# Kernel tuning notes

Hardware: AMD Instinct MI355X
Metric: run time of the kernel (lower is better)

Reference implementation:

```python
import jax, jax.numpy as jnp
import numpy as np


def _unit(h):
    # F.normalize(p=2, dim=-1) equivalent (NormalizeFunc 'unit')
    n = jnp.sqrt(jnp.sum(h * h, axis=-1, keepdims=True))
    return h / jnp.maximum(n, 1e-12)


def setup_inputs() -> dict:
    key = jax.random.key(0)
    k = jax.random.split(key, 6)
    B, T, D, size = 48, 32, 1024, 512
    x = jax.random.normal(k[0], (B, T, D), dtype=jnp.float32)
    w_leaf = jax.random.normal(k[1], (D, size), dtype=jnp.float32) / np.sqrt(D)
    b_leaf = jnp.zeros((size,), dtype=jnp.float32)
    w_comp = jax.random.normal(k[2], (2 * size, size), dtype=jnp.float32) / np.sqrt(2 * size)
    b_comp = jnp.zeros((size,), dtype=jnp.float32)
    s_bilinear = jax.random.normal(k[3], (size, size), dtype=jnp.float32) / np.sqrt(size)
    return {"x": x, "w_leaf": w_leaf, "b_leaf": b_leaf,
            "w_comp": w_comp, "b_comp": b_comp, "s_bilinear": s_bilinear}


def reference(x, w_leaf, b_leaf, w_comp, b_comp, s_bilinear):
    B, T, D = x.shape
    size = w_leaf.shape[1]
    # chart offsets: level lv occupies offsets[lv] : offsets[lv] + (T - lv)
    offsets = np.concatenate([[0], np.cumsum(T - np.arange(T))]).astype(np.int64)
    ncells = T * (T + 1) // 2

    # leaf_transform: MLP + unit normalization
    leaf = _unit(jax.nn.relu(x @ w_leaf + b_leaf))  # [B, T, size]
    chart_h = jnp.zeros((B, ncells, size), x.dtype).at[:, :T].set(leaf)
    chart_s = jnp.zeros((B, ncells, 1), x.dtype)

    for level in range(1, T):
        L = T - level  # spans at this level
        N = level      # split points per span
        pos = np.arange(L)[:, None]
        n = np.arange(N)[None, :]
        # left child: level n at pos; right child: level (level-n-1) at pos+n+1
        l_idx = offsets[n] + pos                       # [L, N]
        r_idx = offsets[level - n - 1] + pos + n + 1   # [L, N]

        lh = chart_h[:, l_idx]  # [B, L, N, size]
        rh = chart_h[:, r_idx]  # [B, L, N, size]
        ls = chart_s[:, l_idx]  # [B, L, N, 1]
        rs = chart_s[:, r_idx]  # [B, L, N, 1]

        # inside_compose: MLP over concatenated children
        h = jax.nn.relu(jnp.concatenate([lh, rh], axis=-1) @ w_comp + b_comp)
        # inside_score: bilinear compatibility
        xs = jnp.einsum('blnd,de,blne->bln', lh, s_bilinear, rh)[..., None]
        s = xs + ls + rs                  # [B, L, N, 1]
        p = jax.nn.softmax(s, axis=2)
        hbar = _unit(jnp.sum(h * p, axis=2))  # [B, L, size]
        sbar = jnp.sum(s * p, axis=2)         # [B, L, 1]

        off = int(offsets[level])
        chart_h = chart_h.at[:, off:off + L].set(hbar)
        chart_s = chart_s.at[:, off:off + L].set(sbar)

    return chart_h
```

## Files before the change

### kernel.cpp

```cpp
#include <hip/hip_runtime.h>
#include <math.h>

#define BB 48
#define TT 32
#define DD 1024
#define SZ 512
#define NCELLS 528

typedef unsigned short u16;
typedef unsigned int u32;
typedef __attribute__((ext_vector_type(8))) short bf16x8;
typedef __attribute__((ext_vector_type(4))) float f32x4;

__device__ __forceinline__ int off_of(int k) { return TT * k - (k * (k - 1)) / 2; }

__device__ __forceinline__ u16 f2bf(float x) {
    u32 u = __float_as_uint(x);
    u32 r = (u + 0x7fffu + ((u >> 16) & 1u)) >> 16;
    return (u16)r;
}
__device__ __forceinline__ float bf2f(u16 h) {
    return __uint_as_float(((u32)h) << 16);
}
__device__ __forceinline__ u32 pack2(u16 a, u16 b) {
    return (u32)a | ((u32)b << 16);
}
__device__ __forceinline__ float2 upk(u32 v) {
    return make_float2(__uint_as_float(v << 16),
                       __uint_as_float(v & 0xffff0000u));
}

__global__ __launch_bounds__(256) void prep_w(
    const float* __restrict__ w_comp, const float* __restrict__ s_bil,
    u16* __restrict__ WT)
{
    int idx = blockIdx.x * 256 + threadIdx.x;
    int n = idx >> 9, k = idx & 511;
    float w;
    if (n < 512)       w = w_comp[(size_t)k * SZ + n];
    else if (n < 1024) w = w_comp[(size_t)(512 + k) * SZ + (n - 512)];
    else               w = s_bil[(size_t)k * SZ + (n - 1024)];
    WT[idx] = f2bf(w);
}

__global__ __launch_bounds__(256) void prep_wl(
    const float* __restrict__ w_leaf,
    u16* __restrict__ WLT_hi, u16* __restrict__ WLT_lo)
{
    int idx = blockIdx.x * 256 + threadIdx.x;
    int n = idx >> 10, k = idx & 1023;
    float w = w_leaf[(size_t)k * SZ + n];
    u16 hi = f2bf(w);
    u16 lo = f2bf(w - bf2f(hi));
    WLT_hi[idx] = hi;
    WLT_lo[idx] = lo;
}

__global__ __launch_bounds__(256) void leaf_mfma(
    const float* __restrict__ x,
    const u16* __restrict__ WLT_hi, const u16* __restrict__ WLT_lo,
    const float* __restrict__ b_leaf, float* __restrict__ leaf_pre)
{
    __shared__ u16 Ah[128][40];
    __shared__ u16 Bh[64][40], Bl[64][40];

    const int col0 = blockIdx.x * 64;
    const int row0 = blockIdx.y * 128;
    const int t = threadIdx.x;

    const int srow = t >> 1, skh = (t & 1) * 16;
    const float* ap = x + (size_t)(row0 + srow) * DD + skh;
    const int bcol = t >> 2, bch = (t & 3) * 8;
    const u16* bph = WLT_hi + (size_t)(col0 + bcol) * DD + bch;
    const u16* bpl = WLT_lo + (size_t)(col0 + bcol) * DD + bch;

    const int lane = t & 63, wv = t >> 6;
    const int wr = wv >> 1, wc = wv & 1;
    const int l15 = lane & 15, lko = (lane >> 4) * 8;

    f32x4 acc[4][2];
    #pragma unroll
    for (int i = 0; i < 4; ++i)
        #pragma unroll
        for (int j = 0; j < 2; ++j)
            #pragma unroll
            for (int e = 0; e < 4; ++e) acc[i][j][e] = 0.f;

    float4 pa[4];
    uint4 pbh, pbl;
    #pragma unroll
    for (int c = 0; c < 4; ++c) pa[c] = *(const float4*)(ap + c * 4);
    pbh = *(const uint4*)bph;
    pbl = *(const uint4*)bpl;

    for (int k0 = 0; k0 < DD; k0 += 32) {
        u32 wh[8];
        #pragma unroll
        for (int c = 0; c < 4; ++c) {
            wh[c * 2]     = pack2(f2bf(pa[c].x), f2bf(pa[c].y));
            wh[c * 2 + 1] = pack2(f2bf(pa[c].z), f2bf(pa[c].w));
        }
        *(uint4*)&Ah[srow][skh]     = make_uint4(wh[0], wh[1], wh[2], wh[3]);
        *(uint4*)&Ah[srow][skh + 8] = make_uint4(wh[4], wh[5], wh[6], wh[7]);
        *(uint4*)&Bh[bcol][bch] = pbh;
        *(uint4*)&Bl[bcol][bch] = pbl;
        __syncthreads();

        if (k0 + 32 < DD) {
            #pragma unroll
            for (int c = 0; c < 4; ++c)
                pa[c] = *(const float4*)(ap + k0 + 32 + c * 4);
            pbh = *(const uint4*)(bph + k0 + 32);
            pbl = *(const uint4*)(bpl + k0 + 32);
        }

        bf16x8 fah[4], fbh[2], fbl[2];
        #pragma unroll
        for (int i = 0; i < 4; ++i)
            fah[i] = *(const bf16x8*)&Ah[wr * 64 + i * 16 + l15][lko];
        #pragma unroll
        for (int j = 0; j < 2; ++j) {
            fbh[j] = *(const bf16x8*)&Bh[wc * 32 + j * 16 + l15][lko];
            fbl[j] = *(const bf16x8*)&Bl[wc * 32 + j * 16 + l15][lko];
        }
        #pragma unroll
        for (int i = 0; i < 4; ++i) {
            #pragma unroll
            for (int j = 0; j < 2; ++j) {
                acc[i][j] = __builtin_amdgcn_mfma_f32_16x16x32_bf16(
                    fah[i], fbh[j], acc[i][j], 0, 0, 0);
                acc[i][j] = __builtin_amdgcn_mfma_f32_16x16x32_bf16(
                    fah[i], fbl[j], acc[i][j], 0, 0, 0);
            }
        }
        __syncthreads();
    }

    #pragma unroll
    for (int i = 0; i < 4; ++i) {
        int rbase = row0 + wr * 64 + i * 16 + (lane >> 4) * 4;
        #pragma unroll
        for (int j = 0; j < 2; ++j) {
            int gc = col0 + wc * 32 + j * 16 + l15;
            float bc = b_leaf[gc];
            #pragma unroll
            for (int q = 0; q < 4; ++q)
                leaf_pre[(size_t)(rbase + q) * SZ + gc] =
                    fmaxf(acc[i][j][q] + bc, 0.f);
        }
    }
}

__global__ __launch_bounds__(256) void leaf_norm(
    const float* __restrict__ leaf_pre, float* __restrict__ chart_h,
    u16* __restrict__ Hchart, float* __restrict__ Sarr)
{
    const int r = blockIdx.x;
    const int b = r >> 5, pos = r & 31;
    const int cell = b * NCELLS + pos;
    const int t = threadIdx.x, lane = t & 63, wave = t >> 6;
    __shared__ float red[4];

    float2 v = *(const float2*)&leaf_pre[(size_t)r * SZ + 2 * t];
    float sq = v.x * v.x + v.y * v.y;
    #pragma unroll
    for (int o = 32; o; o >>= 1) sq += __shfl_xor(sq, o);
    if (lane == 0) red[wave] = sq;
    __syncthreads();
    float nrm = sqrtf(red[0] + red[1] + red[2] + red[3]);
    float inv = 1.f / fmaxf(nrm, 1e-12f);
    v.x *= inv; v.y *= inv;
    *(float2*)&chart_h[(size_t)cell * SZ + 2 * t] = v;
    ((u32*)Hchart)[(size_t)cell * 256 + t] = pack2(f2bf(v.x), f2bf(v.y));
    if (t == 0) Sarr[cell] = 0.f;
}

__global__ __launch_bounds__(256) void transform_mfma(
    const u16* __restrict__ Hchart, const u16* __restrict__ WT,
    const float* __restrict__ b_comp,
    u16* __restrict__ ACU, int level, int nrt)
{
    __shared__ u16 Ah[64][40];
    __shared__ u16 Bh[64][40];
    __shared__ int cidx[64];

    const int L = TT - level, rows = BB * L, off = off_of(level);
    const int id = blockIdx.x;
    const int w = (id & 7) * (3 * nrt) + (id >> 3);
    const int rt = w / 24, ct = w % 24;
    const int col0 = ct * 64;

    const int t = threadIdx.x;
    if (t < 64) {
        int g = rt * 64 + t;
        cidx[t] = (g < rows) ? ((g / L) * NCELLS + off + (g % L)) : -1;
    }

    const int srow = t >> 2, skc = (t & 3) * 8;
    int ga = rt * 64 + srow;
    if (ga >= rows) ga = rows - 1;
    const int acell = (ga / L) * NCELLS + off + (ga % L);
    const u16* aph = Hchart + (size_t)acell * SZ + skc;
    const u16* bph = WT + (size_t)(col0 + srow) * SZ + skc;

    const int lane = t & 63, wv = t >> 6;
    const int wr = wv >> 1, wc = wv & 1;
    const int l15 = lane & 15, lko = (lane >> 4) * 8;

    f32x4 acc[2][2];
    #pragma unroll
    for (int i = 0; i < 2; ++i)
        #pragma unroll
        for (int j = 0; j < 2; ++j)
            #pragma unroll
            for (int e = 0; e < 4; ++e) acc[i][j][e] = 0.f;

    uint4 pah = *(const uint4*)aph;
    uint4 pbh = *(const uint4*)bph;

    for (int k0 = 0; k0 < SZ; k0 += 32) {
        *(uint4*)&Ah[srow][skc] = pah;
        *(uint4*)&Bh[srow][skc] = pbh;
        __syncthreads();

        if (k0 + 32 < SZ) {
            pah = *(const uint4*)(aph + k0 + 32);
            pbh = *(const uint4*)(bph + k0 + 32);
        }

        bf16x8 fah[2], fbh[2];
        #pragma unroll
        for (int i = 0; i < 2; ++i)
            fah[i] = *(const bf16x8*)&Ah[wr * 32 + i * 16 + l15][lko];
        #pragma unroll
        for (int j = 0; j < 2; ++j)
            fbh[j] = *(const bf16x8*)&Bh[wc * 32 + j * 16 + l15][lko];
        #pragma unroll
        for (int i = 0; i < 2; ++i)
            #pragma unroll
            for (int j = 0; j < 2; ++j)
                acc[i][j] = __builtin_amdgcn_mfma_f32_16x16x32_bf16(
                    fah[i], fbh[j], acc[i][j], 0, 0, 0);
        __syncthreads();
    }

    #pragma unroll
    for (int i = 0; i < 2; ++i) {
        int rbase = wr * 32 + i * 16 + (lane >> 4) * 4;
        #pragma unroll
        for (int j = 0; j < 2; ++j) {
            int gc = col0 + wc * 32 + j * 16 + l15;
            float bias = (gc < 512) ? b_comp[gc] : 0.f;
            #pragma unroll
            for (int q = 0; q < 4; ++q) {
                int ci = cidx[rbase + q];
                if (ci >= 0)
                    ACU[(size_t)ci * 1536 + gc] = f2bf(acc[i][j][q] + bias);
            }
        }
    }
}

__global__ __launch_bounds__(512) void combine_kernel(
    float* __restrict__ chart_h, const u16* __restrict__ ACU,
    const u16* __restrict__ Hchart,
    float* __restrict__ Sarr, u16* __restrict__ Hchart_w, int level)
{
    const int L = TT - level, N = level;
    const int cpx = (BB * L) >> 3;
    const int swz = (blockIdx.x & 7) * cpx + (blockIdx.x >> 3);
    const int b = swz / L, pos = swz % L;
    const int off = off_of(level);

    __shared__ float s_lds[32], p_lds[32], spre[32];
    __shared__ int lcell[32], rcell[32];
    __shared__ float hred[8][512];
    __shared__ float red[8];

    const int t = threadIdx.x, lane = t & 63, wv = t >> 6;

    if (t < N) {
        int lc = b * NCELLS + off_of(t) + pos;
        int rc = b * NCELLS + off_of(level - t - 1) + pos + t + 1;
        lcell[t] = lc;
        rcell[t] = rc;
        spre[t] = Sarr[lc] + Sarr[rc];
    }
    __syncthreads();

    for (int n = wv; n < N; n += 8) {
        const u16* u  = ACU + (size_t)lcell[n] * 1536 + 1024;
        const u16* hr = Hchart + (size_t)rcell[n] * SZ;
        uint4 uv = *(const uint4*)&u[lane * 8];
        uint4 hv = *(const uint4*)&hr[lane * 8];
        float d = 0.f;
        {
            float2 a = upk(uv.x), h2 = upk(hv.x);
            d = fmaf(a.x, h2.x, fmaf(a.y, h2.y, d));
        }
        {
            float2 a = upk(uv.y), h2 = upk(hv.y);
            d = fmaf(a.x, h2.x, fmaf(a.y, h2.y, d));
        }
        {
            float2 a = upk(uv.z), h2 = upk(hv.z);
            d = fmaf(a.x, h2.x, fmaf(a.y, h2.y, d));
        }
        {
            float2 a = upk(uv.w), h2 = upk(hv.w);
            d = fmaf(a.x, h2.x, fmaf(a.y, h2.y, d));
        }
        #pragma unroll
        for (int o = 32; o; o >>= 1) d += __shfl_xor(d, o);
        if (lane == 0) s_lds[n] = d + spre[n];
    }
    __syncthreads();

    if (wv == 0) {
        float sv = (lane < N) ? s_lds[lane] : -INFINITY;
        float m = sv;
        #pragma unroll
        for (int o = 32; o; o >>= 1) m = fmaxf(m, __shfl_xor(m, o));
        float e = (lane < N) ? expf(sv - m) : 0.f;
        float sum = e;
        #pragma unroll
        for (int o = 32; o; o >>= 1) sum += __shfl_xor(sum, o);
        float p = e / sum;
        if (lane < N) p_lds[lane] = p;
        float sb = (lane < N) ? sv * p : 0.f;
        #pragma unroll
        for (int o = 32; o; o >>= 1) sb += __shfl_xor(sb, o);
        if (lane == 0) Sarr[(size_t)b * NCELLS + off + pos] = sb;
    }
    __syncthreads();

    float hacc[8];
    #pragma unroll
    for (int q = 0; q < 8; ++q) hacc[q] = 0.f;
    for (int n = wv; n < N; n += 8) {
        const u16* A_ = ACU + (size_t)lcell[n] * 1536;
        const u16* C_ = ACU + (size_t)rcell[n] * 1536 + 512;
        uint4 va = *(const uint4*)&A_[lane * 8];
        uint4 vc = *(const uint4*)&C_[lane * 8];
        float p = p_lds[n];
        const u32 av[4] = {va.x, va.y, va.z, va.w};
        const u32 cv[4] = {vc.x, vc.y, vc.z, vc.w};
        #pragma unroll
        for (int c = 0; c < 4; ++c) {
            float2 a2 = upk(av[c]);
            float2 c2 = upk(cv[c]);
            hacc[c * 2]     = fmaf(p, fmaxf(a2.x + c2.x, 0.f), hacc[c * 2]);
            hacc[c * 2 + 1] = fmaf(p, fmaxf(a2.y + c2.y, 0.f), hacc[c * 2 + 1]);
        }
    }
    *(float4*)&hred[wv][lane * 8]     = *(float4*)&hacc[0];
    *(float4*)&hred[wv][lane * 8 + 4] = *(float4*)&hacc[4];
    __syncthreads();

    float hv = hred[0][t] + hred[1][t] + hred[2][t] + hred[3][t]
             + hred[4][t] + hred[5][t] + hred[6][t] + hred[7][t];

    float sq = hv * hv;
    #pragma unroll
    for (int o = 32; o; o >>= 1) sq += __shfl_xor(sq, o);
    if (lane == 0) red[wv] = sq;
    __syncthreads();
    float nrm = sqrtf(((red[0] + red[1]) + (red[2] + red[3]))
                    + ((red[4] + red[5]) + (red[6] + red[7])));
    float inv = 1.f / fmaxf(nrm, 1e-12f);
    hv *= inv;
    hred[0][t] = hv;
    __syncthreads();
    const int ocell = b * NCELLS + off + pos;
    if (t < 256) {
        float x0 = hred[0][2 * t], x1 = hred[0][2 * t + 1];
        *(float2*)&chart_h[(size_t)ocell * SZ + 2 * t] = make_float2(x0, x1);
        ((u32*)Hchart_w)[(size_t)ocell * 256 + t] = pack2(f2bf(x0), f2bf(x1));
    }
}

extern "C" void kernel_launch(void* const* d_in, const int* in_sizes, int n_in,
                              void* d_out, int out_size, void* d_ws, size_t ws_size,
                              hipStream_t stream)
{
    const float* x      = (const float*)d_in[0];
    const float* w_leaf = (const float*)d_in[1];
    const float* b_leaf = (const float*)d_in[2];
    const float* w_comp = (const float*)d_in[3];
    const float* b_comp = (const float*)d_in[4];
    const float* s_bil  = (const float*)d_in[5];
    float* chart_h = (float*)d_out;

    char* ws = (char*)d_ws;
    u16* ACU    = (u16*)ws;                        ws += (size_t)BB * NCELLS * 1536 * 2;
    u16* Hchart = (u16*)ws;                        ws += (size_t)BB * NCELLS * SZ * 2;
    float* Sarr = (float*)ws;                      ws += (size_t)BB * NCELLS * 4;
    u16* WT     = (u16*)ws;                        ws += (size_t)1536 * SZ * 2;
    u16* WLT_hi = (u16*)ws;                        ws += (size_t)SZ * DD * 2;
    u16* WLT_lo = (u16*)ws;                        ws += (size_t)SZ * DD * 2;
    float* leaf_pre = (float*)ws;                  ws += (size_t)BB * TT * SZ * 4;

    prep_w<<<(1536 * SZ) / 256, 256, 0, stream>>>(w_comp, s_bil, WT);
    prep_wl<<<(SZ * DD) / 256, 256, 0, stream>>>(w_leaf, WLT_hi, WLT_lo);
    leaf_mfma<<<dim3(8, 12), 256, 0, stream>>>(x, WLT_hi, WLT_lo, b_leaf, leaf_pre);
    leaf_norm<<<BB * TT, 256, 0, stream>>>(leaf_pre, chart_h, Hchart, Sarr);

    {
        int nrt = (BB * TT + 63) / 64;
        transform_mfma<<<24 * nrt, 256, 0, stream>>>(
            Hchart, WT, b_comp, ACU, 0, nrt);
    }

    for (int level = 1; level < TT; ++level) {
        int L = TT - level;
        combine_kernel<<<BB * L, 512, 0, stream>>>(
            chart_h, ACU, Hchart, Sarr, Hchart, level);
        if (level < TT - 1) {
            int nrt = (BB * L + 63) / 64;
            transform_mfma<<<24 * nrt, 256, 0, stream>>>(
                Hchart, WT, b_comp, ACU, level, nrt);
        }
    }
}
```

Measured before the change: 640.8 us.

## Merge weight prep kernels, unroll combine loops by two, use nontemporal chart stores

```diff
diff --git a/kernel.cpp b/kernel.cpp
--- a/kernel.cpp
+++ b/kernel.cpp
@@ -11,6 +11,7 @@
 typedef unsigned int u32;
 typedef __attribute__((ext_vector_type(8))) short bf16x8;
 typedef __attribute__((ext_vector_type(4))) float f32x4;
+typedef __attribute__((ext_vector_type(2))) float f32x2;
 
 __device__ __forceinline__ int off_of(int k) { return TT * k - (k * (k - 1)) / 2; }
 
@@ -30,30 +31,28 @@
                        __uint_as_float(v & 0xffff0000u));
 }
 
-__global__ __launch_bounds__(256) void prep_w(
+__global__ __launch_bounds__(256) void prep_all(
     const float* __restrict__ w_comp, const float* __restrict__ s_bil,
-    u16* __restrict__ WT)
+    const float* __restrict__ w_leaf,
+    u16* __restrict__ WT, u16* __restrict__ WLT_hi, u16* __restrict__ WLT_lo)
 {
     int idx = blockIdx.x * 256 + threadIdx.x;
-    int n = idx >> 9, k = idx & 511;
-    float w;
-    if (n < 512)       w = w_comp[(size_t)k * SZ + n];
-    else if (n < 1024) w = w_comp[(size_t)(512 + k) * SZ + (n - 512)];
-    else               w = s_bil[(size_t)k * SZ + (n - 1024)];
-    WT[idx] = f2bf(w);
-}
-
-__global__ __launch_bounds__(256) void prep_wl(
-    const float* __restrict__ w_leaf,
-    u16* __restrict__ WLT_hi, u16* __restrict__ WLT_lo)
-{
-    int idx = blockIdx.x * 256 + threadIdx.x;
-    int n = idx >> 10, k = idx & 1023;
-    float w = w_leaf[(size_t)k * SZ + n];
-    u16 hi = f2bf(w);
-    u16 lo = f2bf(w - bf2f(hi));
-    WLT_hi[idx] = hi;
-    WLT_lo[idx] = lo;
+    if (idx < 1536 * 512) {
+        int n = idx >> 9, k = idx & 511;
+        float w;
+        if (n < 512)       w = w_comp[(size_t)k * SZ + n];
+        else if (n < 1024) w = w_comp[(size_t)(512 + k) * SZ + (n - 512)];
+        else               w = s_bil[(size_t)k * SZ + (n - 1024)];
+        WT[idx] = f2bf(w);
+    } else {
+        int i = idx - 1536 * 512;
+        int n = i >> 10, k = i & 1023;
+        float w = w_leaf[(size_t)k * SZ + n];
+        u16 hi = f2bf(w);
+        u16 lo = f2bf(w - bf2f(hi));
+        WLT_hi[i] = hi;
+        WLT_lo[i] = lo;
+    }
 }
 
 __global__ __launch_bounds__(256) void leaf_mfma(
@@ -170,7 +169,8 @@
     float nrm = sqrtf(red[0] + red[1] + red[2] + red[3]);
     float inv = 1.f / fmaxf(nrm, 1e-12f);
     v.x *= inv; v.y *= inv;
-    *(float2*)&chart_h[(size_t)cell * SZ + 2 * t] = v;
+    f32x2 vv; vv.x = v.x; vv.y = v.y;
+    __builtin_nontemporal_store(vv, (f32x2*)&chart_h[(size_t)cell * SZ + 2 * t]);
     ((u32*)Hchart)[(size_t)cell * 256 + t] = pack2(f2bf(v.x), f2bf(v.y));
     if (t == 0) Sarr[cell] = 0.f;
 }
@@ -288,31 +288,39 @@
     }
     __syncthreads();
 
-    for (int n = wv; n < N; n += 8) {
-        const u16* u  = ACU + (size_t)lcell[n] * 1536 + 1024;
-        const u16* hr = Hchart + (size_t)rcell[n] * SZ;
-        uint4 uv = *(const uint4*)&u[lane * 8];
-        uint4 hv = *(const uint4*)&hr[lane * 8];
-        float d = 0.f;
-        {
-            float2 a = upk(uv.x), h2 = upk(hv.x);
-            d = fmaf(a.x, h2.x, fmaf(a.y, h2.y, d));
-        }
-        {
-            float2 a = upk(uv.y), h2 = upk(hv.y);
-            d = fmaf(a.x, h2.x, fmaf(a.y, h2.y, d));
-        }
-        {
-            float2 a = upk(uv.z), h2 = upk(hv.z);
-            d = fmaf(a.x, h2.x, fmaf(a.y, h2.y, d));
-        }
-        {
-            float2 a = upk(uv.w), h2 = upk(hv.w);
-            d = fmaf(a.x, h2.x, fmaf(a.y, h2.y, d));
-        }
-        #pragma unroll
-        for (int o = 32; o; o >>= 1) d += __shfl_xor(d, o);
-        if (lane == 0) s_lds[n] = d + spre[n];
+    for (int n = wv; n < N; n += 16) {
+        int n2 = n + 8;
+        bool has2 = n2 < N;
+        int nn = has2 ? n2 : n;
+        const u16* u0  = ACU + (size_t)lcell[n] * 1536 + 1024;
+        const u16* hr0 = Hchart + (size_t)rcell[n] * SZ;
+        const u16* u1  = ACU + (size_t)lcell[nn] * 1536 + 1024;
+        const u16* hr1 = Hchart + (size_t)rcell[nn] * SZ;
+        uint4 uv0 = *(const uint4*)&u0[lane * 8];
+        uint4 hv0 = *(const uint4*)&hr0[lane * 8];
+        uint4 uv1 = *(const uint4*)&u1[lane * 8];
+        uint4 hv1 = *(const uint4*)&hr1[lane * 8];
+        const u32 ua[4] = {uv0.x, uv0.y, uv0.z, uv0.w};
+        const u32 ha[4] = {hv0.x, hv0.y, hv0.z, hv0.w};
+        const u32 ub[4] = {uv1.x, uv1.y, uv1.z, uv1.w};
+        const u32 hb[4] = {hv1.x, hv1.y, hv1.z, hv1.w};
+        float d0 = 0.f, d1 = 0.f;
+        #pragma unroll
+        for (int c = 0; c < 4; ++c) {
+            float2 a0 = upk(ua[c]), g0 = upk(ha[c]);
+            float2 a1 = upk(ub[c]), g1 = upk(hb[c]);
+            d0 = fmaf(a0.x, g0.x, fmaf(a0.y, g0.y, d0));
+            d1 = fmaf(a1.x, g1.x, fmaf(a1.y, g1.y, d1));
+        }
+        #pragma unroll
+        for (int o = 32; o; o >>= 1) {
+            d0 += __shfl_xor(d0, o);
+            d1 += __shfl_xor(d1, o);
+        }
+        if (lane == 0) {
+            s_lds[n] = d0 + spre[n];
+            if (has2) s_lds[n2] = d1 + spre[n2];
+        }
     }
     __syncthreads();
 
@@ -337,20 +345,32 @@
     float hacc[8];
     #pragma unroll
     for (int q = 0; q < 8; ++q) hacc[q] = 0.f;
-    for (int n = wv; n < N; n += 8) {
-        const u16* A_ = ACU + (size_t)lcell[n] * 1536;
-        const u16* C_ = ACU + (size_t)rcell[n] * 1536 + 512;
-        uint4 va = *(const uint4*)&A_[lane * 8];
-        uint4 vc = *(const uint4*)&C_[lane * 8];
-        float p = p_lds[n];
-        const u32 av[4] = {va.x, va.y, va.z, va.w};
-        const u32 cv[4] = {vc.x, vc.y, vc.z, vc.w};
+    for (int n = wv; n < N; n += 16) {
+        int n2 = n + 8;
+        bool has2 = n2 < N;
+        int nn = has2 ? n2 : n;
+        const u16* A0 = ACU + (size_t)lcell[n] * 1536;
+        const u16* C0 = ACU + (size_t)rcell[n] * 1536 + 512;
+        const u16* A1 = ACU + (size_t)lcell[nn] * 1536;
+        const u16* C1 = ACU + (size_t)rcell[nn] * 1536 + 512;
+        uint4 va0 = *(const uint4*)&A0[lane * 8];
+        uint4 vc0 = *(const uint4*)&C0[lane * 8];
+        uint4 va1 = *(const uint4*)&A1[lane * 8];
+        uint4 vc1 = *(const uint4*)&C1[lane * 8];
+        float p0 = p_lds[n];
+        float p1 = has2 ? p_lds[n2] : 0.f;
+        const u32 aa[4] = {va0.x, va0.y, va0.z, va0.w};
+        const u32 ca[4] = {vc0.x, vc0.y, vc0.z, vc0.w};
+        const u32 ab[4] = {va1.x, va1.y, va1.z, va1.w};
+        const u32 cb[4] = {vc1.x, vc1.y, vc1.z, vc1.w};
         #pragma unroll
         for (int c = 0; c < 4; ++c) {
-            float2 a2 = upk(av[c]);
-            float2 c2 = upk(cv[c]);
-            hacc[c * 2]     = fmaf(p, fmaxf(a2.x + c2.x, 0.f), hacc[c * 2]);
-            hacc[c * 2 + 1] = fmaf(p, fmaxf(a2.y + c2.y, 0.f), hacc[c * 2 + 1]);
+            float2 x0 = upk(aa[c]), y0 = upk(ca[c]);
+            float2 x1 = upk(ab[c]), y1 = upk(cb[c]);
+            hacc[c * 2]     = fmaf(p0, fmaxf(x0.x + y0.x, 0.f), hacc[c * 2]);
+            hacc[c * 2 + 1] = fmaf(p0, fmaxf(x0.y + y0.y, 0.f), hacc[c * 2 + 1]);
+            hacc[c * 2]     = fmaf(p1, fmaxf(x1.x + y1.x, 0.f), hacc[c * 2]);
+            hacc[c * 2 + 1] = fmaf(p1, fmaxf(x1.y + y1.y, 0.f), hacc[c * 2 + 1]);
         }
     }
     *(float4*)&hred[wv][lane * 8]     = *(float4*)&hacc[0];
@@ -374,7 +394,9 @@
     const int ocell = b * NCELLS + off + pos;
     if (t < 256) {
         float x0 = hred[0][2 * t], x1 = hred[0][2 * t + 1];
-        *(float2*)&chart_h[(size_t)ocell * SZ + 2 * t] = make_float2(x0, x1);
+        f32x2 vv; vv.x = x0; vv.y = x1;
+        __builtin_nontemporal_store(vv,
+            (f32x2*)&chart_h[(size_t)ocell * SZ + 2 * t]);
         ((u32*)Hchart_w)[(size_t)ocell * 256 + t] = pack2(f2bf(x0), f2bf(x1));
     }
 }
@@ -400,8 +422,8 @@
     u16* WLT_lo = (u16*)ws;                        ws += (size_t)SZ * DD * 2;
     float* leaf_pre = (float*)ws;                  ws += (size_t)BB * TT * SZ * 4;
 
-    prep_w<<<(1536 * SZ) / 256, 256, 0, stream>>>(w_comp, s_bil, WT);
-    prep_wl<<<(SZ * DD) / 256, 256, 0, stream>>>(w_leaf, WLT_hi, WLT_lo);
+    prep_all<<<(1536 * 512 + 512 * 1024) / 256, 256, 0, stream>>>(
+        w_comp, s_bil, w_leaf, WT, WLT_hi, WLT_lo);
     leaf_mfma<<<dim3(8, 12), 256, 0, stream>>>(x, WLT_hi, WLT_lo, b_leaf, leaf_pre);
     leaf_norm<<<BB * TT, 256, 0, stream>>>(leaf_pre, chart_h, Hchart, Sarr);
 
```

Result: no change. 629.1 us (median of 2 runs) (-1.8%).
